# Kernel tuning notes

Measured on AMD Instinct MI355X. Metric: run time of the kernel, lower is better.

Reference implementation:

```python
import jax, jax.numpy as jnp
import numpy as np

N_NODES = 100000
NEG_SLOPE = 0.2


def leaky_relu(x):
    return jnp.where(x >= 0, x, NEG_SLOPE * x)


def gat_conv(x, src, dst, W, a_src, a_dst, b, heads, out_ch, concat):
    # x: [N, F_in]; src/dst: [E]; W: [F_in, heads*out_ch]
    n = x.shape[0]
    h = (x @ W).reshape(n, heads, out_ch)                      # [N, H, C]
    s_src = jnp.einsum('nhc,hc->nh', h, a_src)                 # [N, H]
    s_dst = jnp.einsum('nhc,hc->nh', h, a_dst)                 # [N, H]
    e = leaky_relu(s_src[src] + s_dst[dst])                    # [E, H]
    # segment softmax over incoming edges of each dst node
    m = jax.ops.segment_max(e, dst, num_segments=n)            # [N, H]
    m = jnp.where(jnp.isfinite(m), m, 0.0)
    p = jnp.exp(e - m[dst])                                    # [E, H]
    denom = jax.ops.segment_sum(p, dst, num_segments=n)        # [N, H]
    alpha = p / denom[dst]                                     # [E, H]
    out = jax.ops.segment_sum(h[src] * alpha[..., None], dst, num_segments=n)  # [N, H, C]
    if concat:
        out = out.reshape(n, heads * out_ch)
    else:
        out = out.mean(axis=1)
    return out + b


def setup_inputs() -> dict:
    key = jax.random.key(0)
    ks = jax.random.split(key, 10)
    F_in, hidden, heads, n_cls = 128, 32, 8, 40
    n_edges = 1600000
    x = jax.random.normal(ks[0], (N_NODES, F_in), dtype=jnp.float32)
    edge_index = jax.random.randint(ks[1], (2, n_edges), 0, N_NODES, dtype=jnp.int64)
    s = 0.1
    W1 = jax.random.normal(ks[2], (F_in, heads * hidden), dtype=jnp.float32) * s
    att_src1 = jax.random.normal(ks[3], (heads, hidden), dtype=jnp.float32) * s
    att_dst1 = jax.random.normal(ks[4], (heads, hidden), dtype=jnp.float32) * s
    b1 = jnp.zeros((heads * hidden,), dtype=jnp.float32)
    W2 = jax.random.normal(ks[5], (heads * hidden, n_cls), dtype=jnp.float32) * s
    att_src2 = jax.random.normal(ks[6], (1, n_cls), dtype=jnp.float32) * s
    att_dst2 = jax.random.normal(ks[7], (1, n_cls), dtype=jnp.float32) * s
    b2 = jnp.zeros((n_cls,), dtype=jnp.float32)
    return {
        'x': x, 'edge_index': edge_index,
        'W1': W1, 'att_src1': att_src1, 'att_dst1': att_dst1, 'b1': b1,
        'W2': W2, 'att_src2': att_src2, 'att_dst2': att_dst2, 'b2': b2,
    }


def reference(x, edge_index, W1, att_src1, att_dst1, b1, W2, att_src2, att_dst2, b2):
    n = x.shape[0]
    # PyG GATConv default: add self loops
    loop = jnp.arange(n, dtype=edge_index.dtype)
    src = jnp.concatenate([edge_index[0], loop])
    dst = jnp.concatenate([edge_index[1], loop])
    h = gat_conv(x, src, dst, W1, att_src1, att_dst1, b1, heads=8, out_ch=32, concat=True)
    h = jax.nn.relu(h)  # dropout p=0 / eval mode: identity
    out = gat_conv(h, src, dst, W2, att_src2, att_dst2, b2, heads=1, out_ch=40, concat=True)
    return jax.nn.log_softmax(out, axis=1)
```

## Files before the change

kernel.cpp:

```cpp
#include <hip/hip_runtime.h>
#include <hip/hip_bf16.h>
#include <cmath>


typedef unsigned short ushortT;
typedef unsigned int uintT;
typedef unsigned char ucharT;
typedef __attribute__((ext_vector_type(8))) short short8;
typedef __attribute__((ext_vector_type(4))) float float4v;
typedef __attribute__((ext_vector_type(2))) float float2v;

#define LOG2E 1.4426950408889634f

static __device__ __forceinline__ float bflo(uintT u) {
    return __uint_as_float(u << 16);
}
static __device__ __forceinline__ float bfhi(uintT u) {
    return __uint_as_float(u & 0xffff0000u);
}
static __device__ __forceinline__ ushortT f2bf(float f) {
    __hip_bfloat16 h = __float2bfloat16(f);
    return *reinterpret_cast<ushortT*>(&h);
}
static __device__ __forceinline__ uintT pk(float a, float b) {
    return (uintT)f2bf(a) | ((uintT)f2bf(b) << 16);
}
static __device__ __forceinline__ float ub(uintT u, int k) {
    return (float)((u >> (8 * k)) & 0xffu);
}
static __device__ __forceinline__ float lrelu(float e) {
    return 0.6f * e + 0.4f * fabsf(e);
}

#define PREP_BLOCKS 184
#define EPB 4096

__global__ __launch_bounds__(256) void k_prep(const float* __restrict__ W1,
                                              const float* __restrict__ W2,
                                              const float* __restrict__ a1s,
                                              const float* __restrict__ a1d,
                                              ushortT* __restrict__ W1t,
                                              ushortT* __restrict__ W2t) {
    int t = blockIdx.x * 256 + threadIdx.x;
    if (t < 128 * 256) {
        int k = t >> 8, s = t & 255;
        int c = ((s & 15) << 4) | (s >> 4);
        W1t[s * 128 + k] = f2bf(W1[(size_t)k * 256 + c]);
    } else if (t < 128 * 256 + 48 * 256) {
        int q = t - 128 * 256;
        int k = q / 48, c = q - k * 48;
        W2t[c * 256 + k] = (c < 40) ? f2bf(W2[k * 40 + c]) : (ushortT)0;
    } else if (t < 128 * 256 + 48 * 256 + 2048) {
        int q = t - (128 * 256 + 48 * 256);
        int k = q >> 4, j = q & 15;
        int h = j & 7;
        const float* av = ((j < 8) ? a1s : a1d) + h * 32;
        const float* wr = W1 + (size_t)k * 256 + h * 32;
        float s = 0.f;
        #pragma unroll
        for (int c = 0; c < 32; ++c) s += wr[c] * av[c];
        W1t[(256 + j) * 128 + k] = f2bf(s * LOG2E);
    }
}

static __device__ __forceinline__ void dev_gemm1(int slab,
                                                 const float* __restrict__ A,
                                                 const ushortT* __restrict__ Bt,
                                                 ucharT* __restrict__ h1i,
                                                 float* __restrict__ s1cc,
                                                 float* __restrict__ s1d, int M) {
    int lane = threadIdx.x & 63;
    int r0 = slab * 16;
    if (r0 >= M) return;
    int n = lane & 15, q = lane >> 4;
    const float* arow = A + (size_t)(r0 + n) * 128 + q * 8;
    short8 af[4];
    #pragma unroll
    for (int s = 0; s < 4; ++s) {
        float4 v0 = *(const float4*)(arow + s * 32);
        float4 v1 = *(const float4*)(arow + s * 32 + 4);
        short8 a;
        a[0] = (short)f2bf(v0.x); a[1] = (short)f2bf(v0.y);
        a[2] = (short)f2bf(v0.z); a[3] = (short)f2bf(v0.w);
        a[4] = (short)f2bf(v1.x); a[5] = (short)f2bf(v1.y);
        a[6] = (short)f2bf(v1.z); a[7] = (short)f2bf(v1.w);
        af[s] = a;
    }
    float4v acc[17];
    #pragma unroll
    for (int j = 0; j < 17; ++j) acc[j] = (float4v){0.f, 0.f, 0.f, 0.f};
    #pragma unroll
    for (int s = 0; s < 4; ++s) {
        #pragma unroll
        for (int j = 0; j < 17; ++j) {
            short8 b = *(const short8*)(Bt + (size_t)(j * 16 + n) * 128 + s * 32 + q * 8);
            acc[j] = __builtin_amdgcn_mfma_f32_16x16x32_bf16(af[s], b, acc[j], 0, 0, 0);
        }
    }
    float am[4];
    #pragma unroll
    for (int r = 0; r < 4; ++r) {
        float m = 0.f;
        #pragma unroll
        for (int j = 0; j < 16; ++j) m = fmaxf(m, fabsf(acc[j][r]));
        am[r] = m;
    }
    #pragma unroll
    for (int off = 1; off < 16; off <<= 1) {
        #pragma unroll
        for (int r = 0; r < 4; ++r) am[r] = fmaxf(am[r], __shfl_xor(am[r], off, 64));
    }
    #pragma unroll
    for (int r = 0; r < 4; ++r) {
        int row = r0 + q * 4 + r;
        float m = am[r];
        float si = (m > 0.f) ? 127.f / m : 0.f;
        uintT wd[4];
        #pragma unroll
        for (int wq = 0; wq < 4; ++wq) {
            uintT p4 = 0;
            #pragma unroll
            for (int b = 0; b < 4; ++b) {
                int j = wq * 4 + b;
                int qv = (int)rintf(acc[j][r] * si) + 128;
                p4 |= ((uintT)(qv & 0xff)) << (8 * b);
            }
            wd[wq] = p4;
        }
        uint4 o = make_uint4(wd[0], wd[1], wd[2], wd[3]);
        *(uint4*)(h1i + (size_t)row * 256 + n * 16) = o;
        float vv = acc[16][r];
        if (n < 8) {
            *(float2*)(s1cc + ((size_t)row << 4) + n * 2) =
                make_float2(vv, m * (1.f / 127.f));
        } else {
            s1d[(size_t)row * 8 + (n - 8)] = vv;
        }
    }
}

__global__ __launch_bounds__(256) void k_cnt_g1(const int* __restrict__ ei, int E,
                                                int* __restrict__ counts, int nbuck,
                                                const float* __restrict__ A,
                                                const ushortT* __restrict__ Bt,
                                                ucharT* __restrict__ h1i,
                                                float* __restrict__ s1cc,
                                                float* __restrict__ s1d,
                                                int M, int nPrim, int slabBase) {
    if (blockIdx.x >= nPrim) {
        int wave = threadIdx.x >> 6;
        int slab = slabBase + (blockIdx.x - nPrim) * 4 + wave;
        dev_gemm1(slab, A, Bt, h1i, s1cc, s1d, M);
        return;
    }
    __shared__ int h[1024];
    int t = threadIdx.x;
    for (int i = t; i < nbuck; i += 256) h[i] = 0;
    __syncthreads();
    int base = blockIdx.x * EPB;
    #pragma unroll
    for (int r = 0; r < 4; ++r) {
        int i4 = base + (r * 256 + t) * 4;
        if (i4 + 3 < E) {
            int4 d = *(const int4*)(ei + E + i4);
            atomicAdd(&h[d.x >> 7], 1);
            atomicAdd(&h[d.y >> 7], 1);
            atomicAdd(&h[d.z >> 7], 1);
            atomicAdd(&h[d.w >> 7], 1);
        } else {
            for (int j = i4; j < E; ++j) atomicAdd(&h[ei[E + j] >> 7], 1);
        }
    }
    __syncthreads();
    int* crow = counts + (size_t)blockIdx.x * nbuck;
    for (int i = t; i < nbuck; i += 256) crow[i] = h[i];
}

__global__ __launch_bounds__(256) void k_scan_cols(int* __restrict__ counts,
                                                   int* __restrict__ totals,
                                                   int nb1, int nbuck) {
    __shared__ int wsum[4];
    int k = blockIdx.x;
    int t = threadIdx.x, lane = t & 63, wv = t >> 6;
    int e0 = 2 * t, e1 = 2 * t + 1;
    int v0 = (e0 < nb1) ? counts[(size_t)e0 * nbuck + k] : 0;
    int v1 = (e1 < nb1) ? counts[(size_t)e1 * nbuck + k] : 0;
    int s = v0 + v1;
    int incl = s;
    #pragma unroll
    for (int off = 1; off < 64; off <<= 1) {
        int u = __shfl_up(incl, off, 64);
        if (lane >= off) incl += u;
    }
    if (lane == 63) wsum[wv] = incl;
    __syncthreads();
    int add = 0;
    if (wv > 0) add += wsum[0];
    if (wv > 1) add += wsum[1];
    if (wv > 2) add += wsum[2];
    incl += add;
    int excl = incl - s;
    if (e0 < nb1) counts[(size_t)e0 * nbuck + k] = excl;
    if (e1 < nb1) counts[(size_t)e1 * nbuck + k] = excl + v0;
    if (t == 255) totals[k] = incl;
}

__global__ __launch_bounds__(256) void k_place_g1(const int* __restrict__ ei, int E,
                                                  const int* __restrict__ counts,
                                                  const int* __restrict__ totals,
                                                  int* __restrict__ bstart,
                                                  uintT* __restrict__ tmp, int nbuck,
                                                  const float* __restrict__ A,
                                                  const ushortT* __restrict__ Bt,
                                                  ucharT* __restrict__ h1i,
                                                  float* __restrict__ s1cc,
                                                  float* __restrict__ s1d,
                                                  int M, int nPrim, int slabBase) {
    if (blockIdx.x >= nPrim) {
        int wave = threadIdx.x >> 6;
        int slab = slabBase + (blockIdx.x - nPrim) * 4 + wave;
        dev_gemm1(slab, A, Bt, h1i, s1cc, s1d, M);
        return;
    }
    __shared__ int st[1024];
    __shared__ int pos[1024];
    __shared__ int wsum[4];
    int t = threadIdx.x, lane = t & 63, wv = t >> 6;
    int b = blockIdx.x;
    int g[4];
    int s = 0;
    #pragma unroll
    for (int j = 0; j < 4; ++j) {
        int e = 4 * t + j;
        g[j] = (e < nbuck) ? totals[e] : 0;
        s += g[j];
    }
    int incl = s;
    #pragma unroll
    for (int off = 1; off < 64; off <<= 1) {
        int u = __shfl_up(incl, off, 64);
        if (lane >= off) incl += u;
    }
    if (lane == 63) wsum[wv] = incl;
    __syncthreads();
    int add = 0;
    if (wv > 0) add += wsum[0];
    if (wv > 1) add += wsum[1];
    if (wv > 2) add += wsum[2];
    int excl = incl + add - s;
    #pragma unroll
    for (int j = 0; j < 4; ++j) {
        int e = 4 * t + j;
        if (e < nbuck) st[e] = excl;
        excl += g[j];
    }
    __syncthreads();
    const int* crow = counts + (size_t)b * nbuck;
    for (int i = t; i < nbuck; i += 256) {
        int sv = st[i];
        pos[i] = sv + crow[i];
        if (b == 0) bstart[i] = sv;
    }
    __syncthreads();
    int base = b * EPB;
    #pragma unroll
    for (int r = 0; r < 4; ++r) {
        int i4 = base + (r * 256 + t) * 4;
        if (i4 + 3 < E) {
            int4 sv = *(const int4*)(ei + i4);
            int4 dv = *(const int4*)(ei + E + i4);
            int p0 = atomicAdd(&pos[dv.x >> 7], 1);
            tmp[p0] = (uintT)sv.x | (((uintT)dv.x & 127u) << 17);
            int p1 = atomicAdd(&pos[dv.y >> 7], 1);
            tmp[p1] = (uintT)sv.y | (((uintT)dv.y & 127u) << 17);
            int p2 = atomicAdd(&pos[dv.z >> 7], 1);
            tmp[p2] = (uintT)sv.z | (((uintT)dv.z & 127u) << 17);
            int p3 = atomicAdd(&pos[dv.w >> 7], 1);
            tmp[p3] = (uintT)sv.w | (((uintT)dv.w & 127u) << 17);
        } else {
            for (int j = i4; j < E; ++j) {
                int sj = ei[j], dj = ei[E + j];
                int p = atomicAdd(&pos[dj >> 7], 1);
                tmp[p] = (uintT)sj | (((uintT)dj & 127u) << 17);
            }
        }
    }
}

static __device__ __forceinline__ void dev_csr(int k,
                                               const uintT* __restrict__ tmp,
                                               const int* __restrict__ bstart,
                                               const int* __restrict__ totals,
                                               int* __restrict__ rowptr,
                                               int* __restrict__ csr_src,
                                               int N, int* cnt, int* cur,
                                               int* wtot) {
    int t = threadIdx.x;
    int nodeBase = k << 7;
    int nn = N - nodeBase;
    if (nn > 128) nn = 128;
    int myStart = bstart[k];
    int myCount = totals[k];
    int csrBase = myStart + nodeBase;
    if (t < 128) cnt[t] = 0;
    __syncthreads();
    for (int i = t; i < myCount; i += 256) {
        uintT p = tmp[myStart + i];
        atomicAdd(&cnt[p >> 17], 1);
    }
    __syncthreads();
    int dseg = 0, incl = 0;
    if (t < 128) {
        dseg = (t < nn) ? cnt[t] + 1 : 0;
        incl = dseg;
        #pragma unroll
        for (int off = 1; off < 64; off <<= 1) {
            int u = __shfl_up(incl, off, 64);
            if ((t & 63) >= off) incl += u;
        }
        if (t == 63) *wtot = incl;
    }
    __syncthreads();
    if (t < nn) {
        int excl = incl - dseg + ((t >= 64) ? *wtot : 0);
        int rp = csrBase + excl;
        int node = nodeBase + t;
        rowptr[node + 1] = rp + dseg;
        csr_src[rp] = node;
        cur[t] = rp + 1;
    }
    if (k == 0 && t == 0) rowptr[0] = 0;
    __syncthreads();
    for (int i = t; i < myCount; i += 256) {
        uintT p = tmp[myStart + i];
        int ld = p >> 17;
        int q = atomicAdd(&cur[ld], 1);
        csr_src[q] = (int)(p & 0x1FFFFu);
    }
}

__global__ __launch_bounds__(256) void k_csr_g1(const uintT* __restrict__ tmp,
                                                const int* __restrict__ bstart,
                                                const int* __restrict__ totals,
                                                int* __restrict__ rowptr,
                                                int* __restrict__ csr_src,
                                                int N,
                                                const float* __restrict__ A,
                                                const ushortT* __restrict__ Bt,
                                                ucharT* __restrict__ h1i,
                                                float* __restrict__ s1cc,
                                                float* __restrict__ s1d,
                                                int M, int nPrim, int slabBase) {
    __shared__ int cnt[128];
    __shared__ int cur[128];
    __shared__ int wtot;
    if (blockIdx.x >= nPrim) {
        int wave = threadIdx.x >> 6;
        int slab = slabBase + (blockIdx.x - nPrim) * 4 + wave;
        dev_gemm1(slab, A, Bt, h1i, s1cc, s1d, M);
        return;
    }
    dev_csr(blockIdx.x, tmp, bstart, totals, rowptr, csr_src, N, cnt, cur, &wtot);
}

struct Edge1 {
    float2 svc;
    uint4 v;
    int si;
};

static __device__ __forceinline__ void ldi1(Edge1& S, int j, int endm1,
                                            const int* __restrict__ csr_src) {
    int jj = j < endm1 ? j : endm1;
    S.si = csr_src[jj];
}

static __device__ __forceinline__ void ldv1(Edge1& S, int j, int end,
                                            const float2* __restrict__ sc2,
                                            const ucharT* __restrict__ hb, int head) {
    if (j < end) {
        int s = S.si;
        S.svc = sc2[((size_t)s << 3) + head];
        S.v = *(const uint4*)(hb + ((size_t)s << 8));
    }
}

static __device__ __forceinline__ void ac1(const Edge1& S, float sdn,
                                           float2v* A, float& l, float& sps) {
    float p = exp2f(lrelu(S.svc.x + sdn));
    l += p;
    float ps = p * S.svc.y;
    sps += ps;
    float2v p2 = {ps, ps};
    uintT w;
    w = S.v.x;
    A[0] += p2 * (float2v){ub(w, 0), ub(w, 1)};
    A[1] += p2 * (float2v){ub(w, 2), ub(w, 3)};
    w = S.v.y;
    A[2] += p2 * (float2v){ub(w, 0), ub(w, 1)};
    A[3] += p2 * (float2v){ub(w, 2), ub(w, 3)};
    w = S.v.z;
    A[4] += p2 * (float2v){ub(w, 0), ub(w, 1)};
    A[5] += p2 * (float2v){ub(w, 2), ub(w, 3)};
    w = S.v.w;
    A[6] += p2 * (float2v){ub(w, 0), ub(w, 1)};
    A[7] += p2 * (float2v){ub(w, 2), ub(w, 3)};
}

static __device__ __forceinline__ void dev_agg1_pair(int n0, int NN,
                                                     const ucharT* __restrict__ h1i,
                                                     const float* __restrict__ s1cc,
                                                     const float* __restrict__ s1d,
                                                     const int* __restrict__ rowptr,
                                                     const int* __restrict__ csr_src,
                                                     const float* __restrict__ b1,
                                                     ushortT* __restrict__ out1) {
    int lane = threadIdx.x & 63;
    int half = lane >> 5;
    int n = n0 + half;
    bool act = n < NN;
    int l32 = lane & 31;
    int g = l32 >> 4;
    int cl = l32 & 15;
    int head = cl >> 1;
    int beg = 0, end = 0;
    if (act) {
        beg = rowptr[n];
        end = rowptr[n + 1];
    }
    float sdn = act ? s1d[(size_t)n * 8 + head] : 0.f;
    const ucharT* hb = h1i + cl * 16;
    const float2* sc2 = (const float2*)s1cc;
    float2v A[8];
    #pragma unroll
    for (int k = 0; k < 8; ++k) A[k] = (float2v){0.f, 0.f};
    float l = 0.f, sps = 0.f;
    int i0 = beg + g;
    if (i0 < end) {
        int endm1 = end - 1;
        Edge1 S0, S1, S2;
        S0.svc = S1.svc = S2.svc = make_float2(0.f, 0.f);
        S0.v = S1.v = S2.v = make_uint4(0u, 0u, 0u, 0u);
        ldi1(S0, i0, endm1, csr_src);
        ldi1(S1, i0 + 2, endm1, csr_src);
        ldi1(S2, i0 + 4, endm1, csr_src);
        ldv1(S0, i0, end, sc2, hb, head);
        ldv1(S1, i0 + 2, end, sc2, hb, head);
        ldv1(S2, i0 + 4, end, sc2, hb, head);
        ldi1(S0, i0 + 6, endm1, csr_src);
        ldi1(S1, i0 + 8, endm1, csr_src);
        ldi1(S2, i0 + 10, endm1, csr_src);
        for (int idx = i0; idx < end; idx += 6) {
            ac1(S0, sdn, A, l, sps);
            ldv1(S0, idx + 6, end, sc2, hb, head);
            ldi1(S0, idx + 12, endm1, csr_src);
            if (idx + 2 < end) {
                ac1(S1, sdn, A, l, sps);
                ldv1(S1, idx + 8, end, sc2, hb, head);
                ldi1(S1, idx + 14, endm1, csr_src);
            }
            if (idx + 4 < end) {
                ac1(S2, sdn, A, l, sps);
                ldv1(S2, idx + 10, end, sc2, hb, head);
                ldi1(S2, idx + 16, endm1, csr_src);
            }
        }
    }
    l += __shfl_xor(l, 16, 64);
    sps += __shfl_xor(sps, 16, 64);
    #pragma unroll
    for (int k = 0; k < 8; ++k) {
        A[k].x += __shfl_xor(A[k].x, 16, 64);
        A[k].y += __shfl_xor(A[k].y, 16, 64);
    }
    if (g == 0 && act) {
        float inv = 1.f / l;
        float adj = 128.f * sps;
        const float4 bb0 = *(const float4*)(b1 + cl * 16);
        const float4 bb1 = *(const float4*)(b1 + cl * 16 + 4);
        const float4 bb2 = *(const float4*)(b1 + cl * 16 + 8);
        const float4 bb3 = *(const float4*)(b1 + cl * 16 + 12);
        float bbf[16] = {bb0.x, bb0.y, bb0.z, bb0.w, bb1.x, bb1.y, bb1.z, bb1.w,
                         bb2.x, bb2.y, bb2.z, bb2.w, bb3.x, bb3.y, bb3.z, bb3.w};
        uintT o[8];
        #pragma unroll
        for (int k = 0; k < 8; ++k) {
            float x0 = fmaxf((A[k].x - adj) * inv + bbf[2 * k], 0.f);
            float x1 = fmaxf((A[k].y - adj) * inv + bbf[2 * k + 1], 0.f);
            o[k] = pk(x0, x1);
        }
        *(uint4*)(out1 + (size_t)n * 256 + cl * 16) =
            make_uint4(o[0], o[1], o[2], o[3]);
        *(uint4*)(out1 + (size_t)n * 256 + cl * 16 + 8) =
            make_uint4(o[4], o[5], o[6], o[7]);
    }
}

__global__ __launch_bounds__(256) void k_csr_agg1(const uintT* __restrict__ tmp,
                                                  const int* __restrict__ bstart,
                                                  const int* __restrict__ totals,
                                                  int* __restrict__ rowptr,
                                                  int* __restrict__ csr_src,
                                                  int N, int halfB, int nP4,
                                                  const ucharT* __restrict__ h1i,
                                                  const float* __restrict__ s1cc,
                                                  const float* __restrict__ s1d,
                                                  const float* __restrict__ b1,
                                                  ushortT* __restrict__ out1, int H) {
    __shared__ int cnt[128];
    __shared__ int cur[128];
    __shared__ int wtot;
    if (blockIdx.x < nP4) {
        dev_csr(halfB + blockIdx.x, tmp, bstart, totals, rowptr, csr_src, N,
                cnt, cur, &wtot);
        return;
    }
    int n0 = (blockIdx.x - nP4) * 8 + (threadIdx.x >> 6) * 2;
    if (n0 >= H) return;
    dev_agg1_pair(n0, H, h1i, s1cc, s1d, rowptr, csr_src, b1, out1);
}

__global__ __launch_bounds__(256) void k_agg1(const ucharT* __restrict__ h1i,
                                              const float* __restrict__ s1cc,
                                              const float* __restrict__ s1d,
                                              const int* __restrict__ rowptr,
                                              const int* __restrict__ csr_src,
                                              const float* __restrict__ b1,
                                              ushortT* __restrict__ out1,
                                              int base, int N) {
    int n0 = base + blockIdx.x * 8 + (threadIdx.x >> 6) * 2;
    if (n0 >= N) return;
    dev_agg1_pair(n0, N, h1i, s1cc, s1d, rowptr, csr_src, b1, out1);
}

__global__ __launch_bounds__(256) void k_gemm2(const ushortT* __restrict__ X,
                                               const ushortT* __restrict__ Bt,
                                               const float* __restrict__ a2s,
                                               const float* __restrict__ a2d,
                                               ushortT* __restrict__ H2,
                                               float* __restrict__ s2d, int M) {
    int lane = threadIdx.x & 63, wave = threadIdx.x >> 6;
    int slab = blockIdx.x * 4 + wave;
    int r0 = slab * 16;
    if (r0 >= M) return;
    int n = lane & 15, q = lane >> 4;
    const ushortT* xrow = X + (size_t)(r0 + n) * 256 + q * 8;
    float4v acc[3];
    #pragma unroll
    for (int j = 0; j < 3; ++j) acc[j] = (float4v){0.f, 0.f, 0.f, 0.f};
    #pragma unroll
    for (int s = 0; s < 8; ++s) {
        short8 a = *(const short8*)(xrow + s * 32);
        #pragma unroll
        for (int j = 0; j < 3; ++j) {
            short8 b = *(const short8*)(Bt + (size_t)(j * 16 + n) * 256 + s * 32 + q * 8);
            acc[j] = __builtin_amdgcn_mfma_f32_16x16x32_bf16(a, b, acc[j], 0, 0, 0);
        }
    }
    float asv[3], adv[3];
    #pragma unroll
    for (int j = 0; j < 3; ++j) {
        int col = j * 16 + n;
        asv[j] = (col < 40) ? a2s[col] * LOG2E : 0.f;
        adv[j] = (col < 40) ? a2d[col] * LOG2E : 0.f;
    }
    float us[4], ud[4];
    #pragma unroll
    for (int r = 0; r < 4; ++r) {
        us[r] = acc[0][r] * asv[0] + acc[1][r] * asv[1] + acc[2][r] * asv[2];
        ud[r] = acc[0][r] * adv[0] + acc[1][r] * adv[1] + acc[2][r] * adv[2];
    }
    #pragma unroll
    for (int off = 1; off < 16; off <<= 1) {
        #pragma unroll
        for (int r = 0; r < 4; ++r) {
            us[r] += __shfl_xor(us[r], off, 64);
            ud[r] += __shfl_xor(ud[r], off, 64);
        }
    }
    #pragma unroll
    for (int j = 0; j < 3; ++j) {
        int col = j * 16 + n;
        if (col < 40) {
            #pragma unroll
            for (int r = 0; r < 4; ++r)
                H2[(size_t)(r0 + q * 4 + r) * 48 + col] = f2bf(acc[j][r]);
        }
    }
    if (n == 0) {
        #pragma unroll
        for (int r = 0; r < 4; ++r) {
            int row = r0 + q * 4 + r;
            *(float*)(H2 + (size_t)row * 48 + 40) = us[r];
            s2d[row] = ud[r];
        }
    }
}

struct Edge2 {
    float sv;
    uint2 v;
    int si;
};

static __device__ __forceinline__ void ldi2(Edge2& S, int j, int endm1,
                                            const int* __restrict__ csr_src) {
    int jj = j < endm1 ? j : endm1;
    S.si = csr_src[jj];
}

static __device__ __forceinline__ void ldv2(Edge2& S, int j, int end,
                                            const ushortT* __restrict__ h2, int cl) {
    if (j < end) {
        int s = S.si;
        const ushortT* hr = h2 + (size_t)s * 48;
        S.v = *(const uint2*)(hr + cl * 4);
        S.sv = *(const float*)(hr + 40);
    }
}

static __device__ __forceinline__ void ac2(const Edge2& S, float sdn,
                                           float2v& A01, float2v& A23, float& l) {
    float p = exp2f(lrelu(S.sv + sdn));
    l += p;
    float2v p2 = {p, p};
    A01 += p2 * (float2v){bflo(S.v.x), bfhi(S.v.x)};
    A23 += p2 * (float2v){bflo(S.v.y), bfhi(S.v.y)};
}

__global__ __launch_bounds__(256) void k_agg2lsm(const ushortT* __restrict__ h2,
                                                 const float* __restrict__ sd,
                                                 const int* __restrict__ rowptr,
                                                 const int* __restrict__ csr_src,
                                                 const float* __restrict__ b2,
                                                 float* __restrict__ out, int N) {
    int lane = threadIdx.x & 63;
    int wid = threadIdx.x >> 6;
    int n = blockIdx.x * 4 + wid;
    if (n >= N) return;
    int el = lane / 10;
    int cl = lane - el * 10;
    int beg = rowptr[n], end = rowptr[n + 1];
    float sdn = sd[n];
    float2v A01 = (float2v){0.f, 0.f}, A23 = (float2v){0.f, 0.f};
    float l = 0.f;
    if (el < 6) {
        int i0 = beg + el;
        if (i0 < end) {
            int endm1 = end - 1;
            Edge2 S0, S1, S2;
            S0.sv = S1.sv = S2.sv = 0.f;
            S0.v = S1.v = S2.v = make_uint2(0u, 0u);
            ldi2(S0, i0, endm1, csr_src);
            ldi2(S1, i0 + 6, endm1, csr_src);
            ldi2(S2, i0 + 12, endm1, csr_src);
            ldv2(S0, i0, end, h2, cl);
            ldv2(S1, i0 + 6, end, h2, cl);
            ldv2(S2, i0 + 12, end, h2, cl);
            ldi2(S0, i0 + 18, endm1, csr_src);
            ldi2(S1, i0 + 24, endm1, csr_src);
            ldi2(S2, i0 + 30, endm1, csr_src);
            for (int idx = i0; idx < end; idx += 18) {
                ac2(S0, sdn, A01, A23, l);
                ldv2(S0, idx + 18, end, h2, cl);
                ldi2(S0, idx + 36, endm1, csr_src);
                if (idx + 6 < end) {
                    ac2(S1, sdn, A01, A23, l);
                    ldv2(S1, idx + 24, end, h2, cl);
                    ldi2(S1, idx + 42, endm1, csr_src);
                }
                if (idx + 12 < end) {
                    ac2(S2, sdn, A01, A23, l);
                    ldv2(S2, idx + 30, end, h2, cl);
                    ldi2(S2, idx + 48, endm1, csr_src);
                }
            }
        }
    }
    float a0 = A01.x, a1 = A01.y, a2 = A23.x, a3 = A23.y;
    int src = lane + 30;
    if (src > 63) src = 63;
    bool f = (el < 3);
    float u;
    u = __shfl(a0, src, 64); if (f) a0 += u;
    u = __shfl(a1, src, 64); if (f) a1 += u;
    u = __shfl(a2, src, 64); if (f) a2 += u;
    u = __shfl(a3, src, 64); if (f) a3 += u;
    u = __shfl(l, src, 64);  if (f) l += u;
    int s1 = cl + 10, s2 = cl + 20;
    float t0 = a0 + __shfl(a0, s1, 64) + __shfl(a0, s2, 64);
    float t1 = a1 + __shfl(a1, s1, 64) + __shfl(a1, s2, 64);
    float t2 = a2 + __shfl(a2, s1, 64) + __shfl(a2, s2, 64);
    float t3 = a3 + __shfl(a3, s1, 64) + __shfl(a3, s2, 64);
    float lt = l + __shfl(l, s1, 64) + __shfl(l, s2, 64);
    float inv = 1.f / lt;
    float o0 = t0 * inv + b2[cl * 4 + 0];
    float o1 = t1 * inv + b2[cl * 4 + 1];
    float o2 = t2 * inv + b2[cl * 4 + 2];
    float o3 = t3 * inv + b2[cl * 4 + 3];
    float lm = (lane < 10) ? fmaxf(fmaxf(o0, o1), fmaxf(o2, o3)) : -INFINITY;
    #pragma unroll
    for (int off = 32; off; off >>= 1) lm = fmaxf(lm, __shfl_xor(lm, off, 64));
    float le = (lane < 10)
        ? __expf(o0 - lm) + __expf(o1 - lm) + __expf(o2 - lm) + __expf(o3 - lm)
        : 0.f;
    #pragma unroll
    for (int off = 32; off; off >>= 1) le += __shfl_xor(le, off, 64);
    float ls = lm + logf(le);
    if (lane < 10) {
        float4 w = make_float4(o0 - ls, o1 - ls, o2 - ls, o3 - ls);
        *(float4*)(out + (size_t)n * 40 + cl * 4) = w;
    }
}

extern "C" void kernel_launch(void* const* d_in, const int* in_sizes, int n_in,
                              void* d_out, int out_size, void* d_ws, size_t ws_size,
                              hipStream_t stream) {
    const float* x   = (const float*)d_in[0];
    const int*   ei  = (const int*)d_in[1];
    const float* W1  = (const float*)d_in[2];
    const float* a1s = (const float*)d_in[3];
    const float* a1d = (const float*)d_in[4];
    const float* b1  = (const float*)d_in[5];
    const float* W2  = (const float*)d_in[6];
    const float* a2s = (const float*)d_in[7];
    const float* a2d = (const float*)d_in[8];
    const float* b2  = (const float*)d_in[9];
    float* out = (float*)d_out;

    const int N = in_sizes[0] / 128;
    const int E = in_sizes[1] / 2;
    const int ET = E + N;
    const int NBUCK = (N + 127) >> 7;
    const int NB1 = (E + EPB - 1) / EPB;

    char* w = (char*)d_ws;
    ucharT* h1i = (ucharT*)w;
    ushortT* out1b = (ushortT*)(w + (size_t)N * 256);
    int* i_row = (int*)(w + (size_t)N * 768);
    float* s1cc = (float*)(w + (size_t)N * 768 + ((size_t)N + 16) * 4);
    float* s1d = s1cc + (size_t)N * 16;
    int* i_cnt = (int*)(s1d + (size_t)N * 8);
    int* i_tot = i_cnt + (size_t)NB1 * NBUCK;
    int* i_bst = i_tot + NBUCK + 2;
    uintT* i_tmp = (uintT*)(i_bst + NBUCK + 2);
    int* i_csr = (int*)(i_tmp + E);
    ushortT* W1t = (ushortT*)(i_csr + ET);
    ushortT* W2t = W1t + 272 * 128;
    ushortT* h2b = (ushortT*)s1cc;
    float* s2d = (float*)i_cnt;

    const int nb4 = (N + 3) / 4;
    const int nbG = (N / 16 + 3) / 4;
    const int CH  = (nbG + 2) / 3;
    const int halfB = NBUCK >> 1;
    const int H = halfB << 7;
    const int nP4b = NBUCK - halfB;
    const int nAgg1a = (H + 7) / 8;
    const int nAgg1b = (N - H + 7) / 8;

    k_prep<<<PREP_BLOCKS, 256, 0, stream>>>(W1, W2, a1s, a1d, W1t, W2t);
    k_cnt_g1<<<NB1 + CH, 256, 0, stream>>>(ei, E, i_cnt, NBUCK,
                                           x, W1t, h1i, s1cc, s1d,
                                           N, NB1, 0);
    k_scan_cols<<<NBUCK, 256, 0, stream>>>(i_cnt, i_tot, NB1, NBUCK);
    k_place_g1<<<NB1 + CH, 256, 0, stream>>>(ei, E, i_cnt, i_tot, i_bst, i_tmp, NBUCK,
                                             x, W1t, h1i, s1cc, s1d,
                                             N, NB1, CH * 4);
    k_csr_g1<<<halfB + CH, 256, 0, stream>>>(i_tmp, i_bst, i_tot, i_row, i_csr, N,
                                             x, W1t, h1i, s1cc, s1d,
                                             N, halfB, CH * 8);
    k_csr_agg1<<<nP4b + nAgg1a, 256, 0, stream>>>(i_tmp, i_bst, i_tot, i_row, i_csr,
                                                  N, halfB, nP4b,
                                                  h1i, s1cc, s1d, b1, out1b, H);
    k_agg1<<<nAgg1b, 256, 0, stream>>>(h1i, s1cc, s1d, i_row, i_csr, b1,
                                       out1b, H, N);

    k_gemm2<<<nbG, 256, 0, stream>>>(out1b, W2t, a2s, a2d, h2b, s2d, N);
    k_agg2lsm<<<nb4, 256, 0, stream>>>(h2b, s2d, i_row, i_csr, b2, out, N);
}
```

Baseline: 398.8 us.

## Quantize layer-2 features to int8 and overlap first-half GEMM2 with agg1

Layer-2 GEMM output is now stored as per-row-scaled int8 in a 64-byte record, with the source attention score and scale kept alongside. The aggregation subtracts the 128 offset using a scaled probability sum, which cuts gather bytes per edge. GEMM2 for the first half of the nodes is fused into the second-half agg1 launch so the two overlap, and agg2 now handles two nodes per wave instead of one. The int8 quantization adds rounding error to the layer-2 features.

```diff
diff --git a/kernel.cpp b/kernel.cpp
--- a/kernel.cpp
+++ b/kernel.cpp
@@ -12,12 +12,6 @@
 
 #define LOG2E 1.4426950408889634f
 
-static __device__ __forceinline__ float bflo(uintT u) {
-    return __uint_as_float(u << 16);
-}
-static __device__ __forceinline__ float bfhi(uintT u) {
-    return __uint_as_float(u & 0xffff0000u);
-}
 static __device__ __forceinline__ ushortT f2bf(float f) {
     __hip_bfloat16 h = __float2bfloat16(f);
     return *reinterpret_cast<ushortT*>(&h);
@@ -32,7 +26,7 @@
     return 0.6f * e + 0.4f * fabsf(e);
 }
 
-#define PREP_BLOCKS 184
+#define PREP_BLOCKS 200
 #define EPB 4096
 
 __global__ __launch_bounds__(256) void k_prep(const float* __restrict__ W1,
@@ -46,12 +40,14 @@
         int k = t >> 8, s = t & 255;
         int c = ((s & 15) << 4) | (s >> 4);
         W1t[s * 128 + k] = f2bf(W1[(size_t)k * 256 + c]);
-    } else if (t < 128 * 256 + 48 * 256) {
+    } else if (t < 128 * 256 + 64 * 256) {
         int q = t - 128 * 256;
-        int k = q / 48, c = q - k * 48;
-        W2t[c * 256 + k] = (c < 40) ? f2bf(W2[k * 40 + c]) : (ushortT)0;
-    } else if (t < 128 * 256 + 48 * 256 + 2048) {
-        int q = t - (128 * 256 + 48 * 256);
+        int k = q >> 6, s = q & 63;
+        int n = s & 15, j = s >> 4;
+        int c = 4 * n + j;
+        W2t[s * 256 + k] = (n < 10) ? f2bf(W2[k * 40 + c]) : (ushortT)0;
+    } else if (t < 128 * 256 + 64 * 256 + 2048) {
+        int q = t - (128 * 256 + 64 * 256);
         int k = q >> 4, j = q & 15;
         int h = j & 7;
         const float* av = ((j < 8) ? a1s : a1d) + h * 32;
@@ -135,6 +131,83 @@
                 make_float2(vv, m * (1.f / 127.f));
         } else {
             s1d[(size_t)row * 8 + (n - 8)] = vv;
+        }
+    }
+}
+
+static __device__ __forceinline__ void dev_gemm2(int slab,
+                                                 const ushortT* __restrict__ X,
+                                                 const ushortT* __restrict__ Bt,
+                                                 const float* __restrict__ a2s,
+                                                 const float* __restrict__ a2d,
+                                                 ucharT* __restrict__ h2i,
+                                                 float* __restrict__ s2d, int M) {
+    int lane = threadIdx.x & 63;
+    int r0 = slab * 16;
+    if (r0 >= M) return;
+    int n = lane & 15, q = lane >> 4;
+    const ushortT* xrow = X + (size_t)(r0 + n) * 256 + q * 8;
+    float4v acc[4];
+    #pragma unroll
+    for (int j = 0; j < 4; ++j) acc[j] = (float4v){0.f, 0.f, 0.f, 0.f};
+    #pragma unroll
+    for (int s = 0; s < 8; ++s) {
+        short8 a = *(const short8*)(xrow + s * 32);
+        #pragma unroll
+        for (int j = 0; j < 4; ++j) {
+            short8 b = *(const short8*)(Bt + (size_t)(j * 16 + n) * 256 + s * 32 + q * 8);
+            acc[j] = __builtin_amdgcn_mfma_f32_16x16x32_bf16(a, b, acc[j], 0, 0, 0);
+        }
+    }
+    bool vn = (n < 10);
+    float asv[4], adv[4];
+    #pragma unroll
+    for (int j = 0; j < 4; ++j) {
+        int c = 4 * n + j;
+        asv[j] = vn ? a2s[c] * LOG2E : 0.f;
+        adv[j] = vn ? a2d[c] * LOG2E : 0.f;
+    }
+    float us[4], ud[4], am[4];
+    #pragma unroll
+    for (int r = 0; r < 4; ++r) {
+        us[r] = acc[0][r] * asv[0] + acc[1][r] * asv[1] +
+                acc[2][r] * asv[2] + acc[3][r] * asv[3];
+        ud[r] = acc[0][r] * adv[0] + acc[1][r] * adv[1] +
+                acc[2][r] * adv[2] + acc[3][r] * adv[3];
+        float m = 0.f;
+        if (vn) {
+            #pragma unroll
+            for (int j = 0; j < 4; ++j) m = fmaxf(m, fabsf(acc[j][r]));
+        }
+        am[r] = m;
+    }
+    #pragma unroll
+    for (int off = 1; off < 16; off <<= 1) {
+        #pragma unroll
+        for (int r = 0; r < 4; ++r) {
+            us[r] += __shfl_xor(us[r], off, 64);
+            ud[r] += __shfl_xor(ud[r], off, 64);
+            am[r] = fmaxf(am[r], __shfl_xor(am[r], off, 64));
+        }
+    }
+    #pragma unroll
+    for (int r = 0; r < 4; ++r) {
+        int row = r0 + q * 4 + r;
+        float m = am[r];
+        float si = (m > 0.f) ? 127.f / m : 0.f;
+        if (vn) {
+            uintT p4 = 0;
+            #pragma unroll
+            for (int j = 0; j < 4; ++j) {
+                int qv = (int)rintf(acc[j][r] * si) + 128;
+                p4 |= ((uintT)(qv & 0xff)) << (8 * j);
+            }
+            *(uintT*)(h2i + (size_t)row * 64 + n * 4) = p4;
+        }
+        if (n == 0) {
+            *(float2*)(h2i + (size_t)row * 64 + 40) =
+                make_float2(us[r], m * (1.f / 127.f));
+            s2d[row] = ud[r];
         }
     }
 }
@@ -520,14 +593,26 @@
     dev_agg1_pair(n0, H, h1i, s1cc, s1d, rowptr, csr_src, b1, out1);
 }
 
-__global__ __launch_bounds__(256) void k_agg1(const ucharT* __restrict__ h1i,
-                                              const float* __restrict__ s1cc,
-                                              const float* __restrict__ s1d,
-                                              const int* __restrict__ rowptr,
-                                              const int* __restrict__ csr_src,
-                                              const float* __restrict__ b1,
-                                              ushortT* __restrict__ out1,
-                                              int base, int N) {
+__global__ __launch_bounds__(256) void k_agg1_g2(const ucharT* __restrict__ h1i,
+                                                 const float* __restrict__ s1cc,
+                                                 const float* __restrict__ s1d,
+                                                 const int* __restrict__ rowptr,
+                                                 const int* __restrict__ csr_src,
+                                                 const float* __restrict__ b1,
+                                                 ushortT* __restrict__ out1,
+                                                 int base, int N, int nAgg,
+                                                 const ushortT* __restrict__ X,
+                                                 const ushortT* __restrict__ Bt2,
+                                                 const float* __restrict__ a2s,
+                                                 const float* __restrict__ a2d,
+                                                 ucharT* __restrict__ h2i,
+                                                 float* __restrict__ s2d, int MG2) {
+    if (blockIdx.x >= nAgg) {
+        int wave = threadIdx.x >> 6;
+        int slab = (blockIdx.x - nAgg) * 4 + wave;
+        dev_gemm2(slab, X, Bt2, a2s, a2d, h2i, s2d, MG2);
+        return;
+    }
     int n0 = base + blockIdx.x * 8 + (threadIdx.x >> 6) * 2;
     if (n0 >= N) return;
     dev_agg1_pair(n0, N, h1i, s1cc, s1d, rowptr, csr_src, b1, out1);
@@ -537,69 +622,17 @@
                                                const ushortT* __restrict__ Bt,
                                                const float* __restrict__ a2s,
                                                const float* __restrict__ a2d,
-                                               ushortT* __restrict__ H2,
-                                               float* __restrict__ s2d, int M) {
-    int lane = threadIdx.x & 63, wave = threadIdx.x >> 6;
-    int slab = blockIdx.x * 4 + wave;
-    int r0 = slab * 16;
-    if (r0 >= M) return;
-    int n = lane & 15, q = lane >> 4;
-    const ushortT* xrow = X + (size_t)(r0 + n) * 256 + q * 8;
-    float4v acc[3];
-    #pragma unroll
-    for (int j = 0; j < 3; ++j) acc[j] = (float4v){0.f, 0.f, 0.f, 0.f};
-    #pragma unroll
-    for (int s = 0; s < 8; ++s) {
-        short8 a = *(const short8*)(xrow + s * 32);
-        #pragma unroll
-        for (int j = 0; j < 3; ++j) {
-            short8 b = *(const short8*)(Bt + (size_t)(j * 16 + n) * 256 + s * 32 + q * 8);
-            acc[j] = __builtin_amdgcn_mfma_f32_16x16x32_bf16(a, b, acc[j], 0, 0, 0);
-        }
-    }
-    float asv[3], adv[3];
-    #pragma unroll
-    for (int j = 0; j < 3; ++j) {
-        int col = j * 16 + n;
-        asv[j] = (col < 40) ? a2s[col] * LOG2E : 0.f;
-        adv[j] = (col < 40) ? a2d[col] * LOG2E : 0.f;
-    }
-    float us[4], ud[4];
-    #pragma unroll
-    for (int r = 0; r < 4; ++r) {
-        us[r] = acc[0][r] * asv[0] + acc[1][r] * asv[1] + acc[2][r] * asv[2];
-        ud[r] = acc[0][r] * adv[0] + acc[1][r] * adv[1] + acc[2][r] * adv[2];
-    }
-    #pragma unroll
-    for (int off = 1; off < 16; off <<= 1) {
-        #pragma unroll
-        for (int r = 0; r < 4; ++r) {
-            us[r] += __shfl_xor(us[r], off, 64);
-            ud[r] += __shfl_xor(ud[r], off, 64);
-        }
-    }
-    #pragma unroll
-    for (int j = 0; j < 3; ++j) {
-        int col = j * 16 + n;
-        if (col < 40) {
-            #pragma unroll
-            for (int r = 0; r < 4; ++r)
-                H2[(size_t)(r0 + q * 4 + r) * 48 + col] = f2bf(acc[j][r]);
-        }
-    }
-    if (n == 0) {
-        #pragma unroll
-        for (int r = 0; r < 4; ++r) {
-            int row = r0 + q * 4 + r;
-            *(float*)(H2 + (size_t)row * 48 + 40) = us[r];
-            s2d[row] = ud[r];
-        }
-    }
+                                               ucharT* __restrict__ h2i,
+                                               float* __restrict__ s2d,
+                                               int slabBase, int M) {
+    int wave = threadIdx.x >> 6;
+    int slab = slabBase + blockIdx.x * 4 + wave;
+    dev_gemm2(slab, X, Bt, a2s, a2d, h2i, s2d, M);
 }
 
 struct Edge2 {
-    float sv;
-    uint2 v;
+    float2 svc;
+    uintT v;
     int si;
 };
 
@@ -610,104 +643,107 @@
 }
 
 static __device__ __forceinline__ void ldv2(Edge2& S, int j, int end,
-                                            const ushortT* __restrict__ h2, int cl) {
+                                            const ucharT* __restrict__ h2i, int cl) {
     if (j < end) {
-        int s = S.si;
-        const ushortT* hr = h2 + (size_t)s * 48;
-        S.v = *(const uint2*)(hr + cl * 4);
-        S.sv = *(const float*)(hr + 40);
+        const ucharT* hr = h2i + (size_t)S.si * 64;
+        S.v = *(const uintT*)(hr + cl * 4);
+        S.svc = *(const float2*)(hr + 40);
     }
 }
 
 static __device__ __forceinline__ void ac2(const Edge2& S, float sdn,
-                                           float2v& A01, float2v& A23, float& l) {
-    float p = exp2f(lrelu(S.sv + sdn));
+                                           float2v& A01, float2v& A23,
+                                           float& l, float& sps) {
+    float p = exp2f(lrelu(S.svc.x + sdn));
     l += p;
-    float2v p2 = {p, p};
-    A01 += p2 * (float2v){bflo(S.v.x), bfhi(S.v.x)};
-    A23 += p2 * (float2v){bflo(S.v.y), bfhi(S.v.y)};
-}
-
-__global__ __launch_bounds__(256) void k_agg2lsm(const ushortT* __restrict__ h2,
+    float ps = p * S.svc.y;
+    sps += ps;
+    float2v p2 = {ps, ps};
+    A01 += p2 * (float2v){ub(S.v, 0), ub(S.v, 1)};
+    A23 += p2 * (float2v){ub(S.v, 2), ub(S.v, 3)};
+}
+
+__global__ __launch_bounds__(256) void k_agg2lsm(const ucharT* __restrict__ h2i,
                                                  const float* __restrict__ sd,
                                                  const int* __restrict__ rowptr,
                                                  const int* __restrict__ csr_src,
                                                  const float* __restrict__ b2,
                                                  float* __restrict__ out, int N) {
     int lane = threadIdx.x & 63;
-    int wid = threadIdx.x >> 6;
-    int n = blockIdx.x * 4 + wid;
-    if (n >= N) return;
-    int el = lane / 10;
-    int cl = lane - el * 10;
-    int beg = rowptr[n], end = rowptr[n + 1];
-    float sdn = sd[n];
+    int half = lane >> 5;
+    int l32 = lane & 31;
+    int n = blockIdx.x * 8 + (threadIdx.x >> 6) * 2 + half;
+    bool act = n < N;
+    int el = l32 / 10;
+    int cl = l32 - el * 10;
+    int beg = 0, end = 0;
+    if (act) {
+        beg = rowptr[n];
+        end = rowptr[n + 1];
+    }
+    float sdn = act ? sd[n] : 0.f;
     float2v A01 = (float2v){0.f, 0.f}, A23 = (float2v){0.f, 0.f};
-    float l = 0.f;
-    if (el < 6) {
+    float l = 0.f, sps = 0.f;
+    if (el < 3) {
         int i0 = beg + el;
         if (i0 < end) {
             int endm1 = end - 1;
             Edge2 S0, S1, S2;
-            S0.sv = S1.sv = S2.sv = 0.f;
-            S0.v = S1.v = S2.v = make_uint2(0u, 0u);
+            S0.svc = S1.svc = S2.svc = make_float2(0.f, 0.f);
+            S0.v = S1.v = S2.v = 0u;
             ldi2(S0, i0, endm1, csr_src);
-            ldi2(S1, i0 + 6, endm1, csr_src);
-            ldi2(S2, i0 + 12, endm1, csr_src);
-            ldv2(S0, i0, end, h2, cl);
-            ldv2(S1, i0 + 6, end, h2, cl);
-            ldv2(S2, i0 + 12, end, h2, cl);
-            ldi2(S0, i0 + 18, endm1, csr_src);
-            ldi2(S1, i0 + 24, endm1, csr_src);
-            ldi2(S2, i0 + 30, endm1, csr_src);
-            for (int idx = i0; idx < end; idx += 18) {
-                ac2(S0, sdn, A01, A23, l);
-                ldv2(S0, idx + 18, end, h2, cl);
-                ldi2(S0, idx + 36, endm1, csr_src);
+            ldi2(S1, i0 + 3, endm1, csr_src);
+            ldi2(S2, i0 + 6, endm1, csr_src);
+            ldv2(S0, i0, end, h2i, cl);
+            ldv2(S1, i0 + 3, end, h2i, cl);
+            ldv2(S2, i0 + 6, end, h2i, cl);
+            ldi2(S0, i0 + 9, endm1, csr_src);
+            ldi2(S1, i0 + 12, endm1, csr_src);
+            ldi2(S2, i0 + 15, endm1, csr_src);
+            for (int idx = i0; idx < end; idx += 9) {
+                ac2(S0, sdn, A01, A23, l, sps);
+                ldv2(S0, idx + 9, end, h2i, cl);
+                ldi2(S0, idx + 18, endm1, csr_src);
+                if (idx + 3 < end) {
+                    ac2(S1, sdn, A01, A23, l, sps);
+                    ldv2(S1, idx + 12, end, h2i, cl);
+                    ldi2(S1, idx + 21, endm1, csr_src);
+                }
                 if (idx + 6 < end) {
-                    ac2(S1, sdn, A01, A23, l);
-                    ldv2(S1, idx + 24, end, h2, cl);
-                    ldi2(S1, idx + 42, endm1, csr_src);
-                }
-                if (idx + 12 < end) {
-                    ac2(S2, sdn, A01, A23, l);
-                    ldv2(S2, idx + 30, end, h2, cl);
-                    ldi2(S2, idx + 48, endm1, csr_src);
+                    ac2(S2, sdn, A01, A23, l, sps);
+                    ldv2(S2, idx + 15, end, h2i, cl);
+                    ldi2(S2, idx + 24, endm1, csr_src);
                 }
             }
         }
     }
     float a0 = A01.x, a1 = A01.y, a2 = A23.x, a3 = A23.y;
-    int src = lane + 30;
-    if (src > 63) src = 63;
-    bool f = (el < 3);
-    float u;
-    u = __shfl(a0, src, 64); if (f) a0 += u;
-    u = __shfl(a1, src, 64); if (f) a1 += u;
-    u = __shfl(a2, src, 64); if (f) a2 += u;
-    u = __shfl(a3, src, 64); if (f) a3 += u;
-    u = __shfl(l, src, 64);  if (f) l += u;
-    int s1 = cl + 10, s2 = cl + 20;
-    float t0 = a0 + __shfl(a0, s1, 64) + __shfl(a0, s2, 64);
-    float t1 = a1 + __shfl(a1, s1, 64) + __shfl(a1, s2, 64);
-    float t2 = a2 + __shfl(a2, s1, 64) + __shfl(a2, s2, 64);
-    float t3 = a3 + __shfl(a3, s1, 64) + __shfl(a3, s2, 64);
-    float lt = l + __shfl(l, s1, 64) + __shfl(l, s2, 64);
-    float inv = 1.f / lt;
-    float o0 = t0 * inv + b2[cl * 4 + 0];
-    float o1 = t1 * inv + b2[cl * 4 + 1];
-    float o2 = t2 * inv + b2[cl * 4 + 2];
-    float o3 = t3 * inv + b2[cl * 4 + 3];
-    float lm = (lane < 10) ? fmaxf(fmaxf(o0, o1), fmaxf(o2, o3)) : -INFINITY;
-    #pragma unroll
-    for (int off = 32; off; off >>= 1) lm = fmaxf(lm, __shfl_xor(lm, off, 64));
-    float le = (lane < 10)
+    int base = lane & 32;
+    int f1 = base + cl + 10, f2 = base + cl + 20;
+    a0 += __shfl(a0, f1, 64) + __shfl(a0, f2, 64);
+    a1 += __shfl(a1, f1, 64) + __shfl(a1, f2, 64);
+    a2 += __shfl(a2, f1, 64) + __shfl(a2, f2, 64);
+    a3 += __shfl(a3, f1, 64) + __shfl(a3, f2, 64);
+    l  += __shfl(l, f1, 64) + __shfl(l, f2, 64);
+    sps += __shfl(sps, f1, 64) + __shfl(sps, f2, 64);
+    float inv = 1.f / l;
+    float adj = 128.f * sps;
+    float4 bb = *(const float4*)(b2 + cl * 4);
+    float o0 = (a0 - adj) * inv + bb.x;
+    float o1 = (a1 - adj) * inv + bb.y;
+    float o2 = (a2 - adj) * inv + bb.z;
+    float o3 = (a3 - adj) * inv + bb.w;
+    bool valid = (el == 0);
+    float lm = valid ? fmaxf(fmaxf(o0, o1), fmaxf(o2, o3)) : -INFINITY;
+    #pragma unroll
+    for (int off = 16; off; off >>= 1) lm = fmaxf(lm, __shfl_xor(lm, off, 64));
+    float le = valid
         ? __expf(o0 - lm) + __expf(o1 - lm) + __expf(o2 - lm) + __expf(o3 - lm)
         : 0.f;
     #pragma unroll
-    for (int off = 32; off; off >>= 1) le += __shfl_xor(le, off, 64);
+    for (int off = 16; off; off >>= 1) le += __shfl_xor(le, off, 64);
     float ls = lm + logf(le);
-    if (lane < 10) {
+    if (valid && act) {
         float4 w = make_float4(o0 - ls, o1 - ls, o2 - ls, o3 - ls);
         *(float4*)(out + (size_t)n * 40 + cl * 4) = w;
     }
@@ -743,14 +779,14 @@
     int* i_cnt = (int*)(s1d + (size_t)N * 8);
     int* i_tot = i_cnt + (size_t)NB1 * NBUCK;
     int* i_bst = i_tot + NBUCK + 2;
-    uintT* i_tmp = (uintT*)(i_bst + NBUCK + 2);
+    uintT* i_tmp = (uintT*)(((uintptr_t)(i_bst + NBUCK + 2) + 63) &
+                            ~(uintptr_t)63);
     int* i_csr = (int*)(i_tmp + E);
     ushortT* W1t = (ushortT*)(i_csr + ET);
     ushortT* W2t = W1t + 272 * 128;
-    ushortT* h2b = (ushortT*)s1cc;
+    ucharT* h2i = (ucharT*)i_tmp;
     float* s2d = (float*)i_cnt;
 
-    const int nb4 = (N + 3) / 4;
     const int nbG = (N / 16 + 3) / 4;
     const int CH  = (nbG + 2) / 3;
     const int halfB = NBUCK >> 1;
@@ -758,6 +794,11 @@
     const int nP4b = NBUCK - halfB;
     const int nAgg1a = (H + 7) / 8;
     const int nAgg1b = (N - H + 7) / 8;
+    const int g2aSlabs = H / 16;
+    const int g2aBlocks = g2aSlabs / 4;
+    const int nSlab = (N + 15) / 16;
+    const int g2bBlocks = (nSlab - g2aSlabs + 3) / 4;
+    const int nb8 = (N + 7) / 8;
 
     k_prep<<<PREP_BLOCKS, 256, 0, stream>>>(W1, W2, a1s, a1d, W1t, W2t);
     k_cnt_g1<<<NB1 + CH, 256, 0, stream>>>(ei, E, i_cnt, NBUCK,
@@ -773,9 +814,11 @@
     k_csr_agg1<<<nP4b + nAgg1a, 256, 0, stream>>>(i_tmp, i_bst, i_tot, i_row, i_csr,
                                                   N, halfB, nP4b,
                                                   h1i, s1cc, s1d, b1, out1b, H);
-    k_agg1<<<nAgg1b, 256, 0, stream>>>(h1i, s1cc, s1d, i_row, i_csr, b1,
-                                       out1b, H, N);
-
-    k_gemm2<<<nbG, 256, 0, stream>>>(out1b, W2t, a2s, a2d, h2b, s2d, N);
-    k_agg2lsm<<<nb4, 256, 0, stream>>>(h2b, s2d, i_row, i_csr, b2, out, N);
-}
+    k_agg1_g2<<<nAgg1b + g2aBlocks, 256, 0, stream>>>(h1i, s1cc, s1d, i_row, i_csr,
+                                                      b1, out1b, H, N, nAgg1b,
+                                                      out1b, W2t, a2s, a2d,
+                                                      h2i, s2d, H);
+    k_gemm2<<<g2bBlocks, 256, 0, stream>>>(out1b, W2t, a2s, a2d, h2i, s2d,
+                                           g2aSlabs, N);
+    k_agg2lsm<<<nb8, 256, 0, stream>>>(h2i, s2d, i_row, i_csr, b2, out, N);
+}
```

Result: no change. 396.6 us (-0.5%).
